# Kernel optimization log

Measured on AMD Instinct MI355X. Metric: run time of the kernel, lower is better.

The kernel has to match this reference:

```python
import jax, jax.numpy as jnp
import numpy as np
from jax import lax

SUBSAMPLE = 2

def _grect(b, bs):
    # grid rect (inclusive) for int boxes b [N,4]
    return jnp.stack([b[:, 0] // bs, b[:, 1] // bs,
                      (b[:, 2] - 1) // bs, (b[:, 3] - 1) // bs], axis=1)

def _rect_overlap(r, allr):
    # r [N,4], allr [M,4] inclusive grid rects -> [N,M] bool
    return ((r[:, None, 0] <= allr[None, :, 2]) & (allr[None, :, 0] <= r[:, None, 2]) &
            (r[:, None, 1] <= allr[None, :, 3]) & (allr[None, :, 1] <= r[:, None, 3]))

def _forward(boxes_curr, boxes_prev, H, W, HG, WG, bs):
    S = SUBSAMPLE
    Nc, Np = boxes_curr.shape[0], boxes_prev.shape[0]
    Hs, Ws = H // S, W // S
    oc, sc = boxes_curr[:, :4], boxes_curr[:, 4]
    op, sp = boxes_prev[:, :4], boxes_prev[:, 4]
    ic = oc.astype(jnp.int32)            # original int coords
    ip = op.astype(jnp.int32)
    cc = (oc / S).astype(jnp.int32)      # subsampled int coords
    cp = (op / S).astype(jnp.int32)

    # --- pairwise IoU on subsampled boxes (matches get_iou semantics) ---
    a = cc.astype(jnp.float32); b = cp.astype(jnp.float32)
    ix1 = jnp.maximum(a[:, None, 0], b[None, :, 0])
    iy1 = jnp.maximum(a[:, None, 1], b[None, :, 1])
    ix2 = jnp.minimum(a[:, None, 2], b[None, :, 2])
    iy2 = jnp.minimum(a[:, None, 3], b[None, :, 3])
    inter = jnp.clip(ix2 - ix1, 0.0) * jnp.clip(iy2 - iy1, 0.0)
    areaA = (a[:, 2] - a[:, 0]) * (a[:, 3] - a[:, 1])
    areaB = (b[:, 2] - b[:, 0]) * (b[:, 3] - b[:, 1])
    iou = inter / (areaA[:, None] + areaB[None, :] - inter)
    best_iou = jnp.max(iou, axis=1)
    best_j = jnp.argmax(iou, axis=1)     # first max, matches strict '>' loop
    matched = best_iou > 0.0
    ig = 1.0 - best_iou

    # --- grid rects & isolation test ---
    gc, gp = _grect(ic, bs), _grect(ip, bs)
    gpj = gp[best_j]
    union = jnp.stack([jnp.minimum(gc[:, 0], gpj[:, 0]), jnp.minimum(gc[:, 1], gpj[:, 1]),
                       jnp.maximum(gc[:, 2], gpj[:, 2]), jnp.maximum(gc[:, 3], gpj[:, 3])], 1)
    wrect = jnp.where(matched[:, None], union, gc)
    allr = jnp.concatenate([gc, gp], 0)                      # [Nc+Np,4]
    cover_other = _rect_overlap(gc, allr) | (matched[:, None] & _rect_overlap(gpj, allr))
    kk = jnp.arange(Nc + Np)[None, :]
    excl = (kk == jnp.arange(Nc)[:, None]) | (matched[:, None] & (kk == Nc + best_j[:, None]))
    isolated = ~jnp.any(cover_other & ~excl, axis=1)

    big = (ic[:, 3] - ic[:, 1]) >= 100
    val_c = jnp.where(isolated & big & (sc >= 0.7), 2.0, 1.0)
    matched_prev = jnp.any(matched[:, None] & (best_j[:, None] == jnp.arange(Np)[None, :]), axis=0)

    rects_w = jnp.concatenate([wrect, gp], 0)
    vals_w = jnp.concatenate([val_c, jnp.ones((Np,), val_c.dtype)], 0)
    act_w = jnp.concatenate([jnp.ones((Nc,), bool), ~matched_prev], 0)
    yy, xx = jnp.arange(HG), jnp.arange(WG)
    ry = (yy[None, :] >= rects_w[:, 1:2]) & (yy[None, :] <= rects_w[:, 3:4])   # [Nw,HG]
    rx = (xx[None, :] >= rects_w[:, 0:1]) & (xx[None, :] <= rects_w[:, 2:3])   # [Nw,WG]
    cover = act_w[:, None, None] & ry[:, :, None] & rx[:, None, :]
    order = jnp.arange(rects_w.shape[0])
    last = jnp.max(jnp.where(cover, order[:, None, None], -1), axis=0)
    grid_ig = jnp.where(last >= 0, vals_w[jnp.clip(last, 0)], 0.0)[None, None]  # [1,1,HG,WG]

    # --- subsampled mask: scatter-max rect writes (order-independent) ---
    rects_m = jnp.concatenate([cc, cp[best_j], cp], 0)
    vals_m = jnp.concatenate([ig * sc, ig * sp[best_j], sp], 0)
    act_m = jnp.concatenate([jnp.ones((Nc,)), matched.astype(jnp.float32),
                             (~matched_prev).astype(jnp.float32)], 0)
    ys, xs = jnp.arange(Hs), jnp.arange(Ws)
    def step(m, w):
        r, v, a = w
        row = (ys >= r[1]) & (ys < r[3])
        col = (xs >= r[0]) & (xs < r[2])
        m = jnp.maximum(m, jnp.where(row[:, None] & col[None, :], v * a, 0.0))
        return m, None
    m0 = jnp.zeros((Hs, Ws), jnp.float32)
    m, _ = lax.scan(step, m0, (rects_m, vals_m, act_m))
    mask = jnp.repeat(jnp.repeat(m, SUBSAMPLE, axis=0), SUBSAMPLE, axis=1)[None, None]  # nearest x2
    return mask, grid_ig

def setup_inputs() -> dict:
    H, W, HG, WG, bs = 2048, 4096, 16, 32, 128
    def make_boxes(key, n, max_w=400.0, max_h=300.0):
        k1, k2, k3, k4, k5 = jax.random.split(key, 5)
        x1 = jax.random.uniform(k1, (n,), minval=0.0, maxval=W - max_w - 1)
        y1 = jax.random.uniform(k2, (n,), minval=0.0, maxval=H - max_h - 1)
        bw = jax.random.uniform(k3, (n,), minval=8.0, maxval=max_w)
        bh = jax.random.uniform(k4, (n,), minval=8.0, maxval=max_h)
        sc = jax.random.uniform(k5, (n,))
        return jnp.stack([x1, y1, x1 + bw, y1 + bh, sc], axis=1).astype(jnp.float32)
    key = jax.random.key(0)
    kc, kp = jax.random.split(key)
    return {"boxes_curr": make_boxes(kc, 512), "boxes_prev": make_boxes(kp, 512),
            "H": H, "W": W, "HG": HG, "WG": WG, "block_size": bs}

def reference(boxes_curr, boxes_prev, H, W, HG, WG, block_size):
    return _forward(boxes_curr, boxes_prev, H, W, HG, WG, block_size)
```

## Files before the change

kernel.cpp:

```cpp
#include <hip/hip_runtime.h>

constexpr int H  = 2048, W = 4096, HG = 16, WG = 32, BS = 128;
constexpr int S  = 2, Hs = H / S, Ws = W / S;
constexpr int TILE_R = 32, TILE_C = 64;
constexpr int LMAX = 1536;
constexpr int NB   = (Ws / TILE_C) * (Hs / TILE_R);
constexpr unsigned long long MAGIC = 0x9E3779B97F4A7C15ULL;

#define AGT __HIP_MEMORY_SCOPE_AGENT
static __device__ __forceinline__ unsigned long long ld_u64(const unsigned long long* p) {
    return __hip_atomic_load(p, __ATOMIC_RELAXED, AGT);
}
static __device__ __forceinline__ void st_u64(unsigned long long* p, unsigned long long v) {
    __hip_atomic_store(p, v, __ATOMIC_RELAXED, AGT);
}

__global__ __launch_bounds__(256) void k_fused(
    const float* __restrict__ bc, const float* __restrict__ bp,
    int Nc, int Np,
    unsigned long long* __restrict__ pk,
    float* __restrict__ out)
{
    __shared__ int4  Lr[LMAX];
    __shared__ float Lw[LMAX];
    __shared__ unsigned long long pkl[512];
    __shared__ unsigned bits[16];
    __shared__ int cnt, s_iso;
    __shared__ float red_f[4];
    __shared__ int   red_j[4];

    int tid  = threadIdx.x;
    int lane = tid & 63, wv = tid >> 6;

    int i = blockIdx.x;
    if (i < Nc) {
        float x1 = bc[i*5+0], y1 = bc[i*5+1], x2 = bc[i*5+2], y2 = bc[i*5+3], sc = bc[i*5+4];
        float ax1 = (float)(int)(x1*0.5f), ay1 = (float)(int)(y1*0.5f);
        float ax2 = (float)(int)(x2*0.5f), ay2 = (float)(int)(y2*0.5f);
        float areaA = (ax2-ax1)*(ay2-ay1);

        float bi = -1.0f; int bj = 0;
        for (int j = tid; j < Np; j += 256) {
            float bx1 = (float)(int)(bp[j*5+0]*0.5f), by1 = (float)(int)(bp[j*5+1]*0.5f);
            float bx2 = (float)(int)(bp[j*5+2]*0.5f), by2 = (float)(int)(bp[j*5+3]*0.5f);
            float ix1 = fmaxf(ax1,bx1), iy1 = fmaxf(ay1,by1);
            float ix2 = fminf(ax2,bx2), iy2 = fminf(ay2,by2);
            float inter = fmaxf(ix2-ix1,0.0f)*fmaxf(iy2-iy1,0.0f);
            float areaB = (bx2-bx1)*(by2-by1);
            float iou = inter/(areaA+areaB-inter);
            if (iou > bi || (iou == bi && j < bj)) { bi = iou; bj = j; }
        }
        #pragma unroll
        for (int off = 32; off; off >>= 1) {
            float oi = __shfl_xor(bi, off);
            int   oj = __shfl_xor(bj, off);
            if (oi > bi || (oi == bi && oj < bj)) { bi = oi; bj = oj; }
        }
        if (tid == 0) s_iso = 0;
        if (lane == 0) { red_f[wv] = bi; red_j[wv] = bj; }
        __syncthreads();
        bi = red_f[0]; bj = red_j[0];
        #pragma unroll
        for (int w2 = 1; w2 < 4; w2++) {
            float oi = red_f[w2]; int oj = red_j[w2];
            if (oi > bi || (oi == bi && oj < bj)) { bi = oi; bj = oj; }
        }
        bool m = bi > 0.0f;

        int gx1=(int)x1/BS, gy1=(int)y1/BS, gx2=((int)x2-1)/BS, gy2=((int)y2-1)/BS;
        float pjx1=bp[bj*5+0], pjy1=bp[bj*5+1], pjx2=bp[bj*5+2], pjy2=bp[bj*5+3];
        int hx1=(int)pjx1/BS, hy1=(int)pjy1/BS, hx2=((int)pjx2-1)/BS, hy2=((int)pjy2-1)/BS;

        bool bad = false;
        int NT = Nc + Np;
        for (int k = tid; k < NT; k += 256) {
            const float* q = (k < Nc) ? &bc[(size_t)k*5] : &bp[(size_t)(k-Nc)*5];
            int qx1=(int)q[0]/BS, qy1=(int)q[1]/BS, qx2=((int)q[2]-1)/BS, qy2=((int)q[3]-1)/BS;
            bool ov = (gx1<=qx2)&&(qx1<=gx2)&&(gy1<=qy2)&&(qy1<=gy2);
            if (m) ov = ov || ((hx1<=qx2)&&(qx1<=hx2)&&(hy1<=qy2)&&(qy1<=hy2));
            bool excl = (k == i) || (m && k == Nc + bj);
            bad |= (ov && !excl);
        }
        if (__any(bad) && lane == 0) atomicOr(&s_iso, 1);
        __syncthreads();

        if (tid == 0) {
            bool big = ((int)y2 - (int)y1) >= 100;
            bool vc2 = (!s_iso && big && sc >= 0.7f);
            float ig = 1.0f - bi;
            unsigned hi = (unsigned)bj | (m ? 1u<<16 : 0u) | (vc2 ? 1u<<17 : 0u);
            unsigned long long payload = (unsigned long long)__float_as_uint(ig) |
                                         ((unsigned long long)hi << 32);
            st_u64(&pk[2*i], payload);
            asm volatile("s_waitcnt vmcnt(0)" ::: "memory");
            st_u64(&pk[2*i+1], payload ^ MAGIC);
        }
    }

    if (tid < 16) bits[tid] = 0u;
    if (tid == 0) cnt = 0;
    __syncthreads();
    for (int r = tid; r < Nc; r += 256) {
        unsigned long long p, g;
        for (;;) {
            p = ld_u64(&pk[2*r]); g = ld_u64(&pk[2*r+1]);
            if ((p ^ g) == MAGIC) break;
            __builtin_amdgcn_s_sleep(8);
        }
        pkl[r] = p;
        unsigned hi = (unsigned)(p >> 32);
        if ((hi >> 16) & 1u) {
            unsigned bj = hi & 0xFFFFu;
            atomicOr(&bits[bj >> 5], 1u << (bj & 31));
        }
    }
    __syncthreads();

    int tileb = blockIdx.x;
    int bx = (tileb & 31) * TILE_C;
    int by = (tileb >> 5) * TILE_R;
    int NT2 = 2*Nc + Np;
    for (int r = tid; r < NT2; r += 256) {
        int4 q; float w;
        if (r < Nc) {
            q = make_int4((int)(bc[r*5+0]*0.5f),(int)(bc[r*5+1]*0.5f),
                          (int)(bc[r*5+2]*0.5f),(int)(bc[r*5+3]*0.5f));
            w = __uint_as_float((unsigned)pkl[r]) * bc[r*5+4];
        } else if (r < 2*Nc) {
            int ii = r - Nc;
            unsigned long long v = pkl[ii];
            unsigned hi = (unsigned)(v >> 32);
            int bj = (int)(hi & 0xFFFFu);
            bool m = (hi >> 16) & 1u;
            q = make_int4((int)(bp[bj*5+0]*0.5f),(int)(bp[bj*5+1]*0.5f),
                          (int)(bp[bj*5+2]*0.5f),(int)(bp[bj*5+3]*0.5f));
            w = m ? __uint_as_float((unsigned)v) * bp[bj*5+4] : 0.0f;
        } else {
            int j = r - 2*Nc;
            bool mp = (bits[j >> 5] >> (j & 31)) & 1u;
            q = make_int4((int)(bp[j*5+0]*0.5f),(int)(bp[j*5+1]*0.5f),
                          (int)(bp[j*5+2]*0.5f),(int)(bp[j*5+3]*0.5f));
            w = mp ? 0.0f : bp[j*5+4];
        }
        if (w > 0.0f && q.x < bx+TILE_C && q.z > bx && q.y < by+TILE_R && q.w > by) {
            int idx = atomicAdd(&cnt, 1);
            if (idx < LMAX) { Lr[idx] = q; Lw[idx] = w; }
        }
    }
    __syncthreads();

    {
        int n = min(cnt, LMAX);
        int tx = tid & 31;
        int ty = tid >> 5;
        int c0 = bx + tx * 2;
        int r0 = by + ty * 4;
        float mv[4][2];
        #pragma unroll
        for (int rr = 0; rr < 4; rr++) { mv[rr][0] = 0.0f; mv[rr][1] = 0.0f; }
        for (int k = 0; k < n; k++) {
            int4 q = Lr[k];
            float w = Lw[k];
            bool cx0 = (c0     >= q.x) && (c0     < q.z);
            bool cx1 = (c0 + 1 >= q.x) && (c0 + 1 < q.z);
            #pragma unroll
            for (int rr = 0; rr < 4; rr++) {
                int y = r0 + rr;
                bool cy = (y >= q.y) && (y < q.w);
                if (cy && cx0) mv[rr][0] = fmaxf(mv[rr][0], w);
                if (cy && cx1) mv[rr][1] = fmaxf(mv[rr][1], w);
            }
        }
        #pragma unroll
        for (int rr = 0; rr < 4; rr++) {
            int y = r0 + rr;
            float4 v = make_float4(mv[rr][0], mv[rr][0], mv[rr][1], mv[rr][1]);
            *(float4*)&out[(size_t)(2*y)     * W + 2*c0] = v;
            *(float4*)&out[(size_t)(2*y + 1) * W + 2*c0] = v;
        }
    }

    int last = -1;
    if (tileb < HG*WG) {
        int gy = tileb / WG, gx = tileb % WG;
        int NT = Nc + Np;
        for (int r = tid; r < NT; r += 256) {
            int4 q; bool act;
            if (r < Nc) {
                float cx1 = bc[r*5+0], cy1 = bc[r*5+1], cx2 = bc[r*5+2], cy2 = bc[r*5+3];
                int ggx1=(int)cx1/BS, ggy1=(int)cy1/BS, ggx2=((int)cx2-1)/BS, ggy2=((int)cy2-1)/BS;
                unsigned hi = (unsigned)(pkl[r] >> 32);
                if ((hi >> 16) & 1u) {
                    int bj = (int)(hi & 0xFFFFu);
                    int hx1=(int)bp[bj*5+0]/BS, hy1=(int)bp[bj*5+1]/BS;
                    int hx2=((int)bp[bj*5+2]-1)/BS, hy2=((int)bp[bj*5+3]-1)/BS;
                    q = make_int4(min(ggx1,hx1), min(ggy1,hy1), max(ggx2,hx2), max(ggy2,hy2));
                } else {
                    q = make_int4(ggx1,ggy1,ggx2,ggy2);
                }
                act = true;
            } else {
                int j = r - Nc;
                act = !((bits[j >> 5] >> (j & 31)) & 1u);
                q = make_int4((int)bp[j*5+0]/BS, (int)bp[j*5+1]/BS,
                              ((int)bp[j*5+2]-1)/BS, ((int)bp[j*5+3]-1)/BS);
            }
            if (act && gx >= q.x && gx <= q.z && gy >= q.y && gy <= q.w) last = r;
        }
        #pragma unroll
        for (int off = 32; off; off >>= 1) last = max(last, __shfl_xor(last, off));
        if (lane == 0) red_j[wv] = last;
    }
    __syncthreads();

    if (tileb < HG*WG && tid == 0) {
        int g = max(max(red_j[0], red_j[1]), max(red_j[2], red_j[3]));
        float gv = 0.0f;
        if (g >= 0) {
            if (g < Nc) gv = (((unsigned)(pkl[g] >> 32) >> 17) & 1u) ? 2.0f : 1.0f;
            else gv = 1.0f;
        }
        out[(size_t)H*W + tileb] = gv;
    }
}

extern "C" void kernel_launch(void* const* d_in, const int* in_sizes, int n_in,
                              void* d_out, int out_size, void* d_ws, size_t ws_size,
                              hipStream_t stream)
{
    const float* bc = (const float*)d_in[0];
    const float* bp = (const float*)d_in[1];
    int Nc = in_sizes[0] / 5;
    int Np = in_sizes[1] / 5;
    float* out = (float*)d_out;
    unsigned long long* pk = (unsigned long long*)d_ws;

    k_fused<<<NB, 256, 0, stream>>>(bc, bp, Nc, Np, pk, out);
}
```

Measured before the change: 24.50 us.

## Defer isolation test to grid-tile blocks, computing it only for winning boxes

The per-box isolation test (a scan over all Nc+Np boxes) used to run in each of the Nc blocks before publishing that box's payload. It now runs lazily in the grid-output blocks, only for the box that wins each grid cell. This shortens the critical path before the cross-block payload handoff, so the blocks spinning on those payloads are released sooner. In exchange, the grid blocks gain extra work and barriers, and the same box may be tested by several grid cells.

```diff
diff --git a/kernel.cpp b/kernel.cpp
--- a/kernel.cpp
+++ b/kernel.cpp
@@ -25,7 +25,7 @@
     __shared__ float Lw[LMAX];
     __shared__ unsigned long long pkl[512];
     __shared__ unsigned bits[16];
-    __shared__ int cnt, s_iso;
+    __shared__ int cnt, s_iso, s_g;
     __shared__ float red_f[4];
     __shared__ int   red_j[4];
 
@@ -34,7 +34,7 @@
 
     int i = blockIdx.x;
     if (i < Nc) {
-        float x1 = bc[i*5+0], y1 = bc[i*5+1], x2 = bc[i*5+2], y2 = bc[i*5+3], sc = bc[i*5+4];
+        float x1 = bc[i*5+0], y1 = bc[i*5+1], x2 = bc[i*5+2], y2 = bc[i*5+3];
         float ax1 = (float)(int)(x1*0.5f), ay1 = (float)(int)(y1*0.5f);
         float ax2 = (float)(int)(x2*0.5f), ay2 = (float)(int)(y2*0.5f);
         float areaA = (ax2-ax1)*(ay2-ay1);
@@ -56,39 +56,18 @@
             int   oj = __shfl_xor(bj, off);
             if (oi > bi || (oi == bi && oj < bj)) { bi = oi; bj = oj; }
         }
-        if (tid == 0) s_iso = 0;
         if (lane == 0) { red_f[wv] = bi; red_j[wv] = bj; }
         __syncthreads();
-        bi = red_f[0]; bj = red_j[0];
-        #pragma unroll
-        for (int w2 = 1; w2 < 4; w2++) {
-            float oi = red_f[w2]; int oj = red_j[w2];
-            if (oi > bi || (oi == bi && oj < bj)) { bi = oi; bj = oj; }
-        }
-        bool m = bi > 0.0f;
-
-        int gx1=(int)x1/BS, gy1=(int)y1/BS, gx2=((int)x2-1)/BS, gy2=((int)y2-1)/BS;
-        float pjx1=bp[bj*5+0], pjy1=bp[bj*5+1], pjx2=bp[bj*5+2], pjy2=bp[bj*5+3];
-        int hx1=(int)pjx1/BS, hy1=(int)pjy1/BS, hx2=((int)pjx2-1)/BS, hy2=((int)pjy2-1)/BS;
-
-        bool bad = false;
-        int NT = Nc + Np;
-        for (int k = tid; k < NT; k += 256) {
-            const float* q = (k < Nc) ? &bc[(size_t)k*5] : &bp[(size_t)(k-Nc)*5];
-            int qx1=(int)q[0]/BS, qy1=(int)q[1]/BS, qx2=((int)q[2]-1)/BS, qy2=((int)q[3]-1)/BS;
-            bool ov = (gx1<=qx2)&&(qx1<=gx2)&&(gy1<=qy2)&&(qy1<=gy2);
-            if (m) ov = ov || ((hx1<=qx2)&&(qx1<=hx2)&&(hy1<=qy2)&&(qy1<=hy2));
-            bool excl = (k == i) || (m && k == Nc + bj);
-            bad |= (ov && !excl);
-        }
-        if (__any(bad) && lane == 0) atomicOr(&s_iso, 1);
-        __syncthreads();
-
         if (tid == 0) {
-            bool big = ((int)y2 - (int)y1) >= 100;
-            bool vc2 = (!s_iso && big && sc >= 0.7f);
+            bi = red_f[0]; bj = red_j[0];
+            #pragma unroll
+            for (int w2 = 1; w2 < 4; w2++) {
+                float oi = red_f[w2]; int oj = red_j[w2];
+                if (oi > bi || (oi == bi && oj < bj)) { bi = oi; bj = oj; }
+            }
+            bool m = bi > 0.0f;
             float ig = 1.0f - bi;
-            unsigned hi = (unsigned)bj | (m ? 1u<<16 : 0u) | (vc2 ? 1u<<17 : 0u);
+            unsigned hi = (unsigned)bj | (m ? 1u<<16 : 0u);
             unsigned long long payload = (unsigned long long)__float_as_uint(ig) |
                                          ((unsigned long long)hi << 32);
             st_u64(&pk[2*i], payload);
@@ -180,10 +159,10 @@
         }
     }
 
-    int last = -1;
     if (tileb < HG*WG) {
         int gy = tileb / WG, gx = tileb % WG;
         int NT = Nc + Np;
+        int last = -1;
         for (int r = tid; r < NT; r += 256) {
             int4 q; bool act;
             if (r < Nc) {
@@ -210,17 +189,41 @@
         #pragma unroll
         for (int off = 32; off; off >>= 1) last = max(last, __shfl_xor(last, off));
         if (lane == 0) red_j[wv] = last;
-    }
-    __syncthreads();
-
-    if (tileb < HG*WG && tid == 0) {
-        int g = max(max(red_j[0], red_j[1]), max(red_j[2], red_j[3]));
-        float gv = 0.0f;
-        if (g >= 0) {
-            if (g < Nc) gv = (((unsigned)(pkl[g] >> 32) >> 17) & 1u) ? 2.0f : 1.0f;
-            else gv = 1.0f;
-        }
-        out[(size_t)H*W + tileb] = gv;
+        __syncthreads();
+        if (tid == 0) {
+            s_g = max(max(red_j[0], red_j[1]), max(red_j[2], red_j[3]));
+            s_iso = 0;
+        }
+        __syncthreads();
+        int g = s_g;
+        if (g >= 0 && g < Nc) {
+            float x1 = bc[g*5+0], y1 = bc[g*5+1], x2 = bc[g*5+2], y2 = bc[g*5+3];
+            int gx1=(int)x1/BS, gy1=(int)y1/BS, gx2=((int)x2-1)/BS, gy2=((int)y2-1)/BS;
+            unsigned hi = (unsigned)(pkl[g] >> 32);
+            bool m = (hi >> 16) & 1u;
+            int bj = (int)(hi & 0xFFFFu);
+            int hx1=(int)bp[bj*5+0]/BS, hy1=(int)bp[bj*5+1]/BS;
+            int hx2=((int)bp[bj*5+2]-1)/BS, hy2=((int)bp[bj*5+3]-1)/BS;
+            bool bad = false;
+            int NTk = Nc + Np;
+            for (int k = tid; k < NTk; k += 256) {
+                const float* q = (k < Nc) ? &bc[(size_t)k*5] : &bp[(size_t)(k-Nc)*5];
+                int qx1=(int)q[0]/BS, qy1=(int)q[1]/BS, qx2=((int)q[2]-1)/BS, qy2=((int)q[3]-1)/BS;
+                bool ov = (gx1<=qx2)&&(qx1<=gx2)&&(gy1<=qy2)&&(qy1<=gy2);
+                if (m) ov = ov || ((hx1<=qx2)&&(qx1<=hx2)&&(hy1<=qy2)&&(qy1<=hy2));
+                bool excl = (k == g) || (m && k == Nc + bj);
+                bad |= (ov && !excl);
+            }
+            if (__any(bad) && lane == 0) atomicOr(&s_iso, 1);
+            __syncthreads();
+            if (tid == 0) {
+                bool big = ((int)y2 - (int)y1) >= 100;
+                float sc = bc[g*5+4];
+                out[(size_t)H*W + tileb] = (!s_iso && big && sc >= 0.7f) ? 2.0f : 1.0f;
+            }
+        } else if (tid == 0) {
+            out[(size_t)H*W + tileb] = (g >= Nc) ? 1.0f : 0.0f;
+        }
     }
 }
 
```

New measurement: 23.42 us, median of 2. 1.05x faster.
